# Kernel tuning notes

Measured on AMD Instinct MI355X. Metric: run time of the kernel, lower is better.

## Reference

```python
import jax, jax.numpy as jnp
import numpy as np
import math

EMB = 128
HW = 128

def setup_inputs() -> dict:
    key = jax.random.key(0)
    k_t, k1, k2, k3, k4 = jax.random.split(key, 5)
    B = 8192
    t = jax.random.uniform(k_t, (B,), dtype=jnp.float32)
    s = 1.0 / math.sqrt(EMB)
    W1 = jax.random.uniform(k1, (EMB, EMB), dtype=jnp.float32, minval=-s, maxval=s)
    b1 = jax.random.uniform(k2, (EMB,), dtype=jnp.float32, minval=-s, maxval=s)
    W2 = jax.random.uniform(k3, (EMB, EMB), dtype=jnp.float32, minval=-s, maxval=s)
    b2 = jax.random.uniform(k4, (EMB,), dtype=jnp.float32, minval=-s, maxval=s)
    return {"t": t, "W1": W1, "b1": b1, "W2": W2, "b2": b2}

def reference(t, W1, b1, W2, b2):
    # sinusoidal embedding: 64 log-spaced freqs in [1, 1000]
    freqs = jnp.exp(jnp.linspace(math.log(1.0), math.log(1000.0), EMB // 2)).astype(jnp.float32)
    ang = (2.0 * math.pi) * freqs  # [64]
    phase = t[:, None] * ang[None, :]  # [B, 64]
    emb = jnp.concatenate([jnp.sin(phase), jnp.cos(phase)], axis=-1)  # [B, 128]
    # MLP: Linear -> SiLU -> Linear -> SiLU (torch Linear: x @ W.T + b)
    h = jax.nn.silu(emb @ W1.T + b1)
    h = jax.nn.silu(h @ W2.T + b2)
    # [B,1,1,128] nearest-upsampled to [B,1,128,128]: broadcast along H
    out = jnp.broadcast_to(h[:, None, None, :], (h.shape[0], 1, HW, HW))
    return out
```

## Files before the change

### kernel.cpp

```cpp
#include <hip/hip_runtime.h>
#include <math.h>

typedef float f32x4 __attribute__((ext_vector_type(4)));

__global__ __launch_bounds__(256) void k_mlp(
    const float* __restrict__ t,
    const float* __restrict__ W1, const float* __restrict__ b1,
    const float* __restrict__ W2, const float* __restrict__ b2,
    float* __restrict__ hs)
{
    __shared__ float emb[2][128];
    __shared__ float h1[2][128];
    __shared__ float h2[2][128];

    const int tid  = threadIdx.x;
    const int base = blockIdx.x * 2;

    if (tid < 128) {
        int b = tid >> 6, k = tid & 63;
        double a   = (double)k * (6.907755278982137 / 63.0);
        float freq = (float)exp(a);
        float ang  = 6.2831853071795865f * freq;
        float ph   = t[base + b] * ang;
        float sv, cv;
        sincosf(ph, &sv, &cv);
        emb[b][k]      = sv;
        emb[b][64 + k] = cv;
    }
    __syncthreads();

    const int b  = tid >> 7;
    const int jj = tid & 127;

    {
        float acc = b1[jj];
        const float4* e = (const float4*)emb[b];
        const float4* w = (const float4*)(W1 + jj * 128);
        #pragma unroll
        for (int k4 = 0; k4 < 32; ++k4) {
            float4 wv = w[k4], ev = e[k4];
            acc = fmaf(wv.x, ev.x, acc); acc = fmaf(wv.y, ev.y, acc);
            acc = fmaf(wv.z, ev.z, acc); acc = fmaf(wv.w, ev.w, acc);
        }
        acc = acc / (1.0f + expf(-acc));
        h1[b][jj] = acc;
    }
    __syncthreads();

    {
        float acc = b2[jj];
        const float4* e = (const float4*)h1[b];
        const float4* w = (const float4*)(W2 + jj * 128);
        #pragma unroll
        for (int k4 = 0; k4 < 32; ++k4) {
            float4 wv = w[k4], ev = e[k4];
            acc = fmaf(wv.x, ev.x, acc); acc = fmaf(wv.y, ev.y, acc);
            acc = fmaf(wv.z, ev.z, acc); acc = fmaf(wv.w, ev.w, acc);
        }
        acc = acc / (1.0f + expf(-acc));
        h2[b][jj] = acc;
    }
    __syncthreads();

    hs[(size_t)base * 128 + tid] = (&h2[0][0])[tid];
}

__global__ __launch_bounds__(256) void k_bcast(
    const float* __restrict__ hs, float* __restrict__ out)
{
    const int tid = threadIdx.x;
    const size_t b = blockIdx.x;
    f32x4 v = ((const f32x4*)(hs + b * 128))[tid & 31];
    f32x4* d = (f32x4*)(out + b * 16384);
    #pragma unroll
    for (int c = 0; c < 16; ++c) {
        d[c * 256 + tid] = v;
    }
}

extern "C" void kernel_launch(void* const* d_in, const int* in_sizes, int n_in,
                              void* d_out, int out_size, void* d_ws, size_t ws_size,
                              hipStream_t stream) {
    const float* t  = (const float*)d_in[0];
    const float* W1 = (const float*)d_in[1];
    const float* b1 = (const float*)d_in[2];
    const float* W2 = (const float*)d_in[3];
    const float* b2 = (const float*)d_in[4];
    float* out = (float*)d_out;
    float* hs  = (float*)d_ws;
    const int B = in_sizes[0];

    k_mlp  <<<B / 2, 256, 0, stream>>>(t, W1, b1, W2, b2, hs);
    k_bcast<<<B,     256, 0, stream>>>(hs, out);
}
```

Measured before the change: 644.2 us.

## Process 16 batch rows per MLP block to reuse weight loads across rows

The MLP kernel now handles 16 timesteps per block instead of 2. Each thread keeps 8 accumulators, so every W1/W2 float4 it loads is reused across 8 batch rows, and the final layer writes directly to global memory without a staging buffer. This cuts repeated global and L2 traffic for the weight matrices and the number of blocks, at the cost of more registers and fewer blocks (512). The broadcast kernel, which writes the large output, is unchanged and probably dominates total time.

```diff
diff --git a/kernel.cpp b/kernel.cpp
--- a/kernel.cpp
+++ b/kernel.cpp
@@ -9,15 +9,17 @@
     const float* __restrict__ W2, const float* __restrict__ b2,
     float* __restrict__ hs)
 {
-    __shared__ float emb[2][128];
-    __shared__ float h1[2][128];
-    __shared__ float h2[2][128];
+    __shared__ __attribute__((aligned(16))) float emb[16][128];
+    __shared__ __attribute__((aligned(16))) float h1[16][128];
 
     const int tid  = threadIdx.x;
-    const int base = blockIdx.x * 2;
+    const int base = blockIdx.x * 16;
 
-    if (tid < 128) {
-        int b = tid >> 6, k = tid & 63;
+    #pragma unroll
+    for (int i = 0; i < 4; ++i) {
+        int idx = i * 256 + tid;
+        int b   = idx >> 6;
+        int k   = idx & 63;
         double a   = (double)k * (6.907755278982137 / 63.0);
         float freq = (float)exp(a);
         float ang  = 6.2831853071795865f * freq;
@@ -29,40 +31,59 @@
     }
     __syncthreads();
 
-    const int b  = tid >> 7;
-    const int jj = tid & 127;
+    const int jj   = tid & 127;
+    const int half = tid >> 7;
 
     {
-        float acc = b1[jj];
-        const float4* e = (const float4*)emb[b];
+        float acc[8];
+        float bv = b1[jj];
+        #pragma unroll
+        for (int m = 0; m < 8; ++m) acc[m] = bv;
         const float4* w = (const float4*)(W1 + jj * 128);
         #pragma unroll
         for (int k4 = 0; k4 < 32; ++k4) {
-            float4 wv = w[k4], ev = e[k4];
-            acc = fmaf(wv.x, ev.x, acc); acc = fmaf(wv.y, ev.y, acc);
-            acc = fmaf(wv.z, ev.z, acc); acc = fmaf(wv.w, ev.w, acc);
+            float4 wv = w[k4];
+            #pragma unroll
+            for (int m = 0; m < 8; ++m) {
+                float4 ev = ((const float4*)emb[half * 8 + m])[k4];
+                acc[m] = fmaf(wv.x, ev.x, acc[m]);
+                acc[m] = fmaf(wv.y, ev.y, acc[m]);
+                acc[m] = fmaf(wv.z, ev.z, acc[m]);
+                acc[m] = fmaf(wv.w, ev.w, acc[m]);
+            }
         }
-        acc = acc / (1.0f + expf(-acc));
-        h1[b][jj] = acc;
+        #pragma unroll
+        for (int m = 0; m < 8; ++m) {
+            float a = acc[m];
+            h1[half * 8 + m][jj] = a / (1.0f + expf(-a));
+        }
     }
     __syncthreads();
 
     {
-        float acc = b2[jj];
-        const float4* e = (const float4*)h1[b];
+        float acc[8];
+        float bv = b2[jj];
+        #pragma unroll
+        for (int m = 0; m < 8; ++m) acc[m] = bv;
         const float4* w = (const float4*)(W2 + jj * 128);
         #pragma unroll
         for (int k4 = 0; k4 < 32; ++k4) {
-            float4 wv = w[k4], ev = e[k4];
-            acc = fmaf(wv.x, ev.x, acc); acc = fmaf(wv.y, ev.y, acc);
-            acc = fmaf(wv.z, ev.z, acc); acc = fmaf(wv.w, ev.w, acc);
+            float4 wv = w[k4];
+            #pragma unroll
+            for (int m = 0; m < 8; ++m) {
+                float4 ev = ((const float4*)h1[half * 8 + m])[k4];
+                acc[m] = fmaf(wv.x, ev.x, acc[m]);
+                acc[m] = fmaf(wv.y, ev.y, acc[m]);
+                acc[m] = fmaf(wv.z, ev.z, acc[m]);
+                acc[m] = fmaf(wv.w, ev.w, acc[m]);
+            }
         }
-        acc = acc / (1.0f + expf(-acc));
-        h2[b][jj] = acc;
+        #pragma unroll
+        for (int m = 0; m < 8; ++m) {
+            float a = acc[m];
+            hs[(size_t)(base + half * 8 + m) * 128 + jj] = a / (1.0f + expf(-a));
+        }
     }
-    __syncthreads();
-
-    hs[(size_t)base * 128 + tid] = (&h2[0][0])[tid];
 }
 
 __global__ __launch_bounds__(256) void k_bcast(
@@ -90,6 +111,6 @@
     float* hs  = (float*)d_ws;
     const int B = in_sizes[0];
 
-    k_mlp  <<<B / 2, 256, 0, stream>>>(t, W1, b1, W2, b2, hs);
-    k_bcast<<<B,     256, 0, stream>>>(hs, out);
+    k_mlp  <<<B / 16, 256, 0, stream>>>(t, W1, b1, W2, b2, hs);
+    k_bcast<<<B,      256, 0, stream>>>(hs, out);
 }
```

Result: faster. 549.7 us (-14.7%).
